# Optimization experiments

Measured on AMD Instinct MI355X. Metric: run time of the kernel, lower is better.

The kernel has to match this reference:

```python
import jax, jax.numpy as jnp
import numpy as np

N = 100000      # nodes
E = 1600000     # edges (avg degree 16)
G = 64          # graphs in batch
IN_DIM, HID, C2, C3, HEADS, NCLS = 64, 128, 64, 32, 4, 5
EPS = 1e-5
NEG_SLOPE = 0.2


def setup_inputs() -> dict:
    key = jax.random.key(0)
    ks = jax.random.split(key, 32)

    def w(k, fan_in, shape):
        return jax.random.normal(k, shape, dtype=jnp.float32) * (1.0 / np.sqrt(fan_in))

    x = jax.random.normal(ks[0], (N, IN_DIM), dtype=jnp.float32)
    edge_index = jax.random.randint(ks[1], (2, E), 0, N)
    batch = jnp.sort(jax.random.randint(ks[2], (N,), 0, G))

    inp = {"x": x, "edge_index": edge_index, "batch": batch}
    # GCN layers (PyG GCNConv: weight then symmetric-normalized aggregation, bias after)
    inp.update(W1=w(ks[3], IN_DIM, (IN_DIM, HID)), b1=jnp.zeros((HID,), jnp.float32))
    inp.update(W2=w(ks[4], HID, (HID, C2)), b2=jnp.zeros((C2,), jnp.float32))
    inp.update(W3=w(ks[5], C2, (C2, C3)), b3=jnp.zeros((C3,), jnp.float32))
    # BatchNorm (inference: running stats)
    def bn_params(k, d):
        k1, k2, k3 = jax.random.split(k, 3)
        return (1.0 + 0.1 * jax.random.normal(k1, (d,), jnp.float32),
                0.1 * jax.random.normal(k2, (d,), jnp.float32),
                0.1 * jax.random.normal(k3, (d,), jnp.float32),
                jax.random.uniform(k, (d,), jnp.float32, 0.5, 1.5))
    inp["g1"], inp["be1"], inp["m1"], inp["v1"] = bn_params(ks[6], HID)
    inp["g2"], inp["be2"], inp["m2"], inp["v2"] = bn_params(ks[7], C2)
    inp["g3"], inp["be3"], inp["m3"], inp["v3"] = bn_params(ks[8], C3)
    # GAT (heads=4, out=32, concat=False -> mean over heads)
    inp["Wg"] = w(ks[9], C3, (C3, HEADS * C3))
    inp["ag_s"] = w(ks[10], C3, (HEADS, C3))
    inp["ag_d"] = w(ks[11], C3, (HEADS, C3))
    inp["bg"] = jnp.zeros((C3,), jnp.float32)
    # classifier MLP 32 -> 16 -> 5
    inp["Wc1"] = w(ks[12], C3, (C3, 16)); inp["bc1"] = jnp.zeros((16,), jnp.float32)
    inp["Wc2"] = w(ks[13], 16, (16, NCLS)); inp["bc2"] = jnp.zeros((NCLS,), jnp.float32)
    return inp


def _bn(h, g, be, m, v):
    return (h - m) * jax.lax.rsqrt(v + EPS) * g + be


def reference(x, edge_index, batch,
              W1, b1, g1, be1, m1, v1,
              W2, b2, g2, be2, m2, v2,
              W3, b3, g3, be3, m3, v3,
              Wg, ag_s, ag_d, bg,
              Wc1, bc1, Wc2, bc2):
    n = x.shape[0]
    loop = jnp.arange(n)
    src = jnp.concatenate([edge_index[0], loop])  # add self-loops (PyG default)
    dst = jnp.concatenate([edge_index[1], loop])

    # GCN symmetric normalization: deg from dst (col), norm = d^-1/2[src]*d^-1/2[dst]
    deg = jnp.zeros((n,), x.dtype).at[dst].add(1.0)
    dinv = jax.lax.rsqrt(deg)  # deg >= 1 due to self-loops
    norm = (dinv[src] * dinv[dst])[:, None]

    def gcn(h, W, b):
        h = h @ W
        return jax.ops.segment_sum(h[src] * norm, dst, num_segments=n) + b

    h = jax.nn.relu(_bn(gcn(x, W1, b1), g1, be1, m1, v1))
    h = jax.nn.relu(_bn(gcn(h, W2, b2), g2, be2, m2, v2))
    h = jax.nn.relu(_bn(gcn(h, W3, b3), g3, be3, m3, v3))

    # GAT: per-edge attention, segment softmax over incoming edges per dst
    hh = (h @ Wg).reshape(n, HEADS, C3)          # [N,H,D]
    a_s = jnp.einsum('nhd,hd->nh', hh, ag_s)     # [N,H]
    a_d = jnp.einsum('nhd,hd->nh', hh, ag_d)
    e = jax.nn.leaky_relu(a_s[src] + a_d[dst], NEG_SLOPE)  # [Eall,H]
    emax = jax.lax.stop_gradient(jax.ops.segment_max(e, dst, num_segments=n))
    ee = jnp.exp(e - emax[dst])
    den = jax.ops.segment_sum(ee, dst, num_segments=n)
    att = ee / den[dst]                          # [Eall,H]
    agg = jax.ops.segment_sum(att[:, :, None] * hh[src], dst, num_segments=n)
    h = jax.nn.relu(agg.mean(axis=1) + bg)       # concat=False -> mean heads

    # global mean pool over graphs
    cnt = jax.ops.segment_sum(jnp.ones((n,), h.dtype), batch, num_segments=G)
    pooled = jax.ops.segment_sum(h, batch, num_segments=G) / jnp.maximum(cnt, 1.0)[:, None]

    # classifier (dropout inactive in eval)
    out = jax.nn.relu(pooled @ Wc1 + bc1) @ Wc2 + bc2
    return out
```

## Files before the change

### kernel.cpp

```cpp
#include <hip/hip_runtime.h>

#define EPSN   1e-5f
#define NEGS   0.2f
#define NGRAPH 64
#define BSHIFT 9
#define NPBK   512
#define GCAP   96

typedef _Float16 half_t;
typedef _Float16 halfv8 __attribute__((ext_vector_type(8)));
typedef _Float16 halfv4 __attribute__((ext_vector_type(4)));
typedef _Float16 halfv2 __attribute__((ext_vector_type(2)));

__device__ __forceinline__ float lrelu(float e) { return e > 0.f ? e : NEGS * e; }

__global__ void k_bin_count(const int* __restrict__ ed, int* __restrict__ bsize,
                            int E, int NB) {
    __shared__ int lcnt[1024];
    for (int i = threadIdx.x; i < NB; i += 256) lcnt[i] = 0;
    __syncthreads();
    int chunk = (E + gridDim.x - 1) / gridDim.x;
    int lo = blockIdx.x * chunk;
    int hi = min(E, lo + chunk);
    for (int e = lo + threadIdx.x; e < hi; e += 256)
        atomicAdd(&lcnt[ed[e] >> BSHIFT], 1);
    __syncthreads();
    for (int b = threadIdx.x; b < NB; b += 256)
        if (lcnt[b]) atomicAdd(&bsize[b], lcnt[b]);
}
__global__ void k_bucket_scan(const int* __restrict__ bsize, int* __restrict__ bbase,
                              int* __restrict__ gcur, int NB) {
    int lane = threadIdx.x;
    if (lane >= 64) return;
    int carry = 0;
    int rounds = (NB + 63) / 64;
    for (int r = 0; r < rounds; ++r) {
        int idx = r * 64 + lane;
        int orig = (idx < NB) ? bsize[idx] : 0;
        int v = orig;
#pragma unroll
        for (int o = 1; o < 64; o <<= 1) {
            int t = __shfl_up(v, o, 64);
            if (lane >= o) v += t;
        }
        if (idx < NB) {
            int excl = carry + v - orig;
            bbase[idx] = excl;
            gcur[idx] = excl;
        }
        carry += __shfl(v, 63, 64);
    }
}
__global__ void k_bin_write(const int* __restrict__ es, const int* __restrict__ ed,
                            int* __restrict__ gcur, unsigned* __restrict__ binned,
                            int E, int NB) {
    __shared__ int lcnt[1024];
    __shared__ int lofs[1024];
    int chunk = (E + gridDim.x - 1) / gridDim.x;
    int lo = blockIdx.x * chunk;
    int hi = min(E, lo + chunk);
    for (int i = threadIdx.x; i < NB; i += 256) lcnt[i] = 0;
    __syncthreads();
    for (int e = lo + threadIdx.x; e < hi; e += 256)
        atomicAdd(&lcnt[ed[e] >> BSHIFT], 1);
    __syncthreads();
    for (int b = threadIdx.x; b < NB; b += 256) {
        int c = lcnt[b];
        lofs[b] = c ? atomicAdd(&gcur[b], c) : 0;
    }
    __syncthreads();
    for (int i = threadIdx.x; i < NB; i += 256) lcnt[i] = 0;
    __syncthreads();
    for (int e = lo + threadIdx.x; e < hi; e += 256) {
        int s = es[e], t = ed[e];
        int b = t >> BSHIFT;
        int pos = lofs[b] + atomicAdd(&lcnt[b], 1);
        binned[pos] = ((unsigned)s << BSHIFT) | (unsigned)(t & (NPBK - 1));
    }
}
__global__ void k_csr_build(const unsigned* __restrict__ binned, const int* __restrict__ bbase,
                            const int* __restrict__ bsize, int* __restrict__ rowptr,
                            int* __restrict__ deg, float* __restrict__ dinv,
                            int* __restrict__ csrc, int N) {
    __shared__ int cnt_l[NPBK];
    __shared__ int ofs_l[NPBK];
    int b = blockIdx.x;
    int base = bbase[b];
    int cnt = bsize[b];
    int nlo = b << BSHIFT;
    int nhi = min(N, nlo + NPBK);
    int nv = nhi - nlo;
    int csrbase = base + nlo;
    int tid = threadIdx.x;
    for (int i = tid; i < NPBK; i += 256) cnt_l[i] = (i < nv) ? 1 : 0;
    __syncthreads();
    for (int e = tid; e < cnt; e += 256)
        atomicAdd(&cnt_l[binned[base + e] & (NPBK - 1)], 1);
    __syncthreads();
    if (tid < 64) {
        int carry = 0;
#pragma unroll
        for (int r = 0; r < NPBK / 64; ++r) {
            int idx = r * 64 + tid;
            int orig = cnt_l[idx];
            int v = orig;
#pragma unroll
            for (int o = 1; o < 64; o <<= 1) {
                int t = __shfl_up(v, o, 64);
                if (tid >= o) v += t;
            }
            ofs_l[idx] = carry + v - orig;
            carry += __shfl(v, 63, 64);
        }
    }
    __syncthreads();
    for (int i = tid; i < nv; i += 256) {
        int node = nlo + i;
        int d = cnt_l[i];
        rowptr[node] = csrbase + ofs_l[i];
        deg[node] = d;
        dinv[node] = rsqrtf((float)d);
    }
    __syncthreads();
    for (int i = tid; i < NPBK; i += 256) cnt_l[i] = ofs_l[i];
    __syncthreads();
    for (int e = tid; e < cnt; e += 256) {
        unsigned u = binned[base + e];
        int p = atomicAdd(&cnt_l[u & (NPBK - 1)], 1);
        csrc[csrbase + p] = (int)(u >> BSHIFT);
    }
    for (int i = tid; i < nv; i += 256) {
        int p = atomicAdd(&cnt_l[i], 1);
        csrc[csrbase + p] = nlo + i;
    }
}

__global__ void k_cvt_xh(const float* __restrict__ x, const float* __restrict__ dinv,
                         half_t* __restrict__ xh, int n) {
    int total = n * 8;
    for (int q = blockIdx.x * blockDim.x + threadIdx.x; q < total;
         q += gridDim.x * blockDim.x) {
        float din = dinv[q >> 3];
        float4 a = ((const float4*)x)[q * 2];
        float4 b = ((const float4*)x)[q * 2 + 1];
        halfv8 h;
        h[0] = (half_t)(a.x * din); h[1] = (half_t)(a.y * din);
        h[2] = (half_t)(a.z * din); h[3] = (half_t)(a.w * din);
        h[4] = (half_t)(b.x * din); h[5] = (half_t)(b.y * din);
        h[6] = (half_t)(b.z * din); h[7] = (half_t)(b.w * din);
        ((halfv8*)xh)[q] = h;
    }
}

template <int K, int M, int EPI>
__global__ void k_matmulh(const half_t* __restrict__ X, const float* __restrict__ W,
                          half_t* __restrict__ Y, int n,
                          const float* __restrict__ b, const float* __restrict__ g,
                          const float* __restrict__ be, const float* __restrict__ m,
                          const float* __restrict__ v, const float* __restrict__ dinv) {
    __shared__ float Wl[K * M];
    for (int i = threadIdx.x; i < K * M / 4; i += 256)
        ((float4*)Wl)[i] = ((const float4*)W)[i];
    __syncthreads();
    const int TPR = M / 4;
    const int RPB = 256 / TPR;
    const int c4  = (threadIdx.x % TPR) * 4;
    int row = blockIdx.x * RPB + threadIdx.x / TPR;
    if (row >= n) return;
    const halfv8* xr = (const halfv8*)(X + (long long)row * K);
    float4 acc = make_float4(0.f, 0.f, 0.f, 0.f);
#pragma unroll
    for (int k8 = 0; k8 < K / 8; ++k8) {
        halfv8 xv = xr[k8];
#pragma unroll
        for (int j = 0; j < 8; ++j) {
            float xs = (float)xv[j];
            float4 wv = *(const float4*)&Wl[(k8 * 8 + j) * M + c4];
            acc.x += xs * wv.x; acc.y += xs * wv.y;
            acc.z += xs * wv.z; acc.w += xs * wv.w;
        }
    }
    if (EPI == 1) {
        float4 bb = *(const float4*)(b + c4);
        float4 mm = *(const float4*)(m + c4);
        float4 vv = *(const float4*)(v + c4);
        float4 gg = *(const float4*)(g + c4);
        float4 ee = *(const float4*)(be + c4);
        acc.x = fmaxf((acc.x + bb.x - mm.x) * rsqrtf(vv.x + EPSN) * gg.x + ee.x, 0.f);
        acc.y = fmaxf((acc.y + bb.y - mm.y) * rsqrtf(vv.y + EPSN) * gg.y + ee.y, 0.f);
        acc.z = fmaxf((acc.z + bb.z - mm.z) * rsqrtf(vv.z + EPSN) * gg.z + ee.z, 0.f);
        acc.w = fmaxf((acc.w + bb.w - mm.w) * rsqrtf(vv.w + EPSN) * gg.w + ee.w, 0.f);
    } else {
        float din = dinv[row];
        acc.x *= din; acc.y *= din; acc.z *= din; acc.w *= din;
    }
    halfv4 hv;
    hv[0] = (half_t)acc.x; hv[1] = (half_t)acc.y;
    hv[2] = (half_t)acc.z; hv[3] = (half_t)acc.w;
    *(halfv4*)(Y + (long long)row * M + c4) = hv;
}

template <int M, int EPI>
__global__ void k_agg4h(const half_t* __restrict__ A, const int* __restrict__ rowptr,
                        const int* __restrict__ deg, const int* __restrict__ csrc,
                        const float* __restrict__ dinv,
                        const float* __restrict__ b, const float* __restrict__ g,
                        const float* __restrict__ be, const float* __restrict__ m,
                        const float* __restrict__ v,
                        half_t* __restrict__ B, int n) {
    const int LPE = M / 8;
    const int EPW = 64 / LPE;
    int node = blockIdx.x * 4 + (threadIdx.x >> 6);
    if (node >= n) return;
    int lane = threadIdx.x & 63;
    int eg = lane / LPE;
    int dl = lane % LPE;
    int beg = rowptr[node];
    int end = beg + deg[node];
    float acc[8];
#pragma unroll
    for (int j = 0; j < 8; ++j) acc[j] = 0.f;
    int i = beg + eg;
    for (; i + EPW < end; i += 2 * EPW) {
        int s0 = csrc[i];
        int s1 = csrc[i + EPW];
        halfv8 x0 = *(const halfv8*)(A + (long long)s0 * M + dl * 8);
        halfv8 x1 = *(const halfv8*)(A + (long long)s1 * M + dl * 8);
#pragma unroll
        for (int j = 0; j < 8; ++j) acc[j] += (float)x0[j] + (float)x1[j];
    }
    if (i < end) {
        int s = csrc[i];
        halfv8 xv = *(const halfv8*)(A + (long long)s * M + dl * 8);
#pragma unroll
        for (int j = 0; j < 8; ++j) acc[j] += (float)xv[j];
    }
#pragma unroll
    for (int off = LPE; off < 64; off <<= 1) {
#pragma unroll
        for (int j = 0; j < 8; ++j) acc[j] += __shfl_xor(acc[j], off);
    }
    if (eg == 0) {
        float din = dinv[node];
        int d0 = dl * 8;
        float o[8];
#pragma unroll
        for (int j = 0; j < 8; ++j) o[j] = acc[j] * din;
        if (EPI == 1) {
#pragma unroll
            for (int j = 0; j < 8; ++j) {
                int d = d0 + j;
                o[j] = fmaxf((o[j] + b[d] - m[d]) * rsqrtf(v[d] + EPSN) * g[d] + be[d], 0.f);
            }
        }
        halfv8 hw;
#pragma unroll
        for (int j = 0; j < 8; ++j) hw[j] = (half_t)o[j];
        *(halfv8*)(B + (long long)node * M + d0) = hw;
    }
}

__global__ void k_wsd(const float* __restrict__ Wg, const float* __restrict__ ags,
                      const float* __restrict__ agd, float* __restrict__ wsd) {
    int j = threadIdx.x;
    if (j < 128) {
        int k = j >> 2, h = j & 3;
        float ss = 0.f, dd = 0.f;
        for (int d2 = 0; d2 < 32; ++d2) {
            float wv = Wg[k * 128 + h * 32 + d2];
            ss += wv * ags[h * 32 + d2];
            dd += wv * agd[h * 32 + d2];
        }
        wsd[j] = ss;
        wsd[128 + j] = dd;
    }
}

__global__ void k_agg_att(const half_t* __restrict__ A, const int* __restrict__ rowptr,
                          const int* __restrict__ deg, const int* __restrict__ csrc,
                          const float* __restrict__ dinv,
                          const float* __restrict__ b, const float* __restrict__ g,
                          const float* __restrict__ be, const float* __restrict__ m,
                          const float* __restrict__ v, const float* __restrict__ wsd,
                          half_t* __restrict__ H3h, float* __restrict__ a_s,
                          float* __restrict__ a_d, int n) {
    __shared__ float Wl[256];
    for (int i = threadIdx.x; i < 256; i += 256) Wl[i] = wsd[i];
    __syncthreads();
    const int M = 32, EPW = 16;
    int node = blockIdx.x * 4 + (threadIdx.x >> 6);
    if (node >= n) return;
    int lane = threadIdx.x & 63;
    int eg = lane >> 2;
    int dl = lane & 3;
    int beg = rowptr[node];
    int end = beg + deg[node];
    float acc[8];
#pragma unroll
    for (int j = 0; j < 8; ++j) acc[j] = 0.f;
    int i = beg + eg;
    for (; i + EPW < end; i += 2 * EPW) {
        int s0 = csrc[i];
        int s1 = csrc[i + EPW];
        halfv8 x0 = *(const halfv8*)(A + (long long)s0 * M + dl * 8);
        halfv8 x1 = *(const halfv8*)(A + (long long)s1 * M + dl * 8);
#pragma unroll
        for (int j = 0; j < 8; ++j) acc[j] += (float)x0[j] + (float)x1[j];
    }
    if (i < end) {
        int s = csrc[i];
        halfv8 xv = *(const halfv8*)(A + (long long)s * M + dl * 8);
#pragma unroll
        for (int j = 0; j < 8; ++j) acc[j] += (float)xv[j];
    }
#pragma unroll
    for (int off = 4; off < 64; off <<= 1) {
#pragma unroll
        for (int j = 0; j < 8; ++j) acc[j] += __shfl_xor(acc[j], off);
    }
    float din = dinv[node];
    int d0 = dl * 8;
    float hv[8];
#pragma unroll
    for (int j = 0; j < 8; ++j) {
        int d = d0 + j;
        hv[j] = fmaxf((acc[j] * din + b[d] - m[d]) * rsqrtf(v[d] + EPSN) * g[d] + be[d], 0.f);
    }
    if (eg == 0) {
        halfv8 hw;
#pragma unroll
        for (int j = 0; j < 8; ++j) hw[j] = (half_t)hv[j];
        *(halfv8*)(H3h + (long long)node * M + d0) = hw;
    }
    int h = lane & 3, sel = (lane >> 2) & 1;
    const float* wp = &Wl[sel * 128];
    float o = 0.f;
#pragma unroll
    for (int src = 0; src < 4; ++src) {
#pragma unroll
        for (int j = 0; j < 8; ++j) {
            float xv = __shfl(hv[j], src);
            o += xv * wp[(src * 8 + j) * 4 + h];
        }
    }
    if (lane < 4) a_s[node * 4 + h] = o;
    else if (lane < 8) a_d[node * 4 + h] = o;
}

__global__ void k_gat4(const half_t* __restrict__ H3h, const float* __restrict__ a_s,
                       const float* __restrict__ a_d, const int* __restrict__ rowptr,
                       const int* __restrict__ deg, const int* __restrict__ csrc,
                       const float* __restrict__ Wg, const float* __restrict__ bg,
                       float* __restrict__ H4, int n) {
    __shared__ float sc[4][GCAP * 4];
    __shared__ int   srcb[4][GCAP];
    __shared__ float wb[4][128];
    int w = threadIdx.x >> 6;
    int node = blockIdx.x * 4 + w;
    if (node >= n) return;
    int lane = threadIdx.x & 63;
    int beg = rowptr[node];
    int cnt = deg[node];
    bool fits = (cnt <= GCAP);
    float4 ad4 = ((const float4*)a_d)[node];
    float m0 = -1e30f, m1 = -1e30f, m2 = -1e30f, m3 = -1e30f;
    if (fits) {
        for (int e = lane; e < cnt; e += 64) {
            int s = csrc[beg + e];
            srcb[w][e] = s;
            float4 as = ((const float4*)a_s)[s];
            float e0 = lrelu(as.x + ad4.x);
            float e1 = lrelu(as.y + ad4.y);
            float e2 = lrelu(as.z + ad4.z);
            float e3 = lrelu(as.w + ad4.w);
            *(float4*)&sc[w][e * 4] = make_float4(e0, e1, e2, e3);
            m0 = fmaxf(m0, e0); m1 = fmaxf(m1, e1);
            m2 = fmaxf(m2, e2); m3 = fmaxf(m3, e3);
        }
    } else {
        for (int e = lane; e < cnt; e += 64) {
            int s = csrc[beg + e];
            float4 as = ((const float4*)a_s)[s];
            m0 = fmaxf(m0, lrelu(as.x + ad4.x));
            m1 = fmaxf(m1, lrelu(as.y + ad4.y));
            m2 = fmaxf(m2, lrelu(as.z + ad4.z));
            m3 = fmaxf(m3, lrelu(as.w + ad4.w));
        }
    }
#pragma unroll
    for (int o = 1; o < 64; o <<= 1) {
        m0 = fmaxf(m0, __shfl_xor(m0, o));
        m1 = fmaxf(m1, __shfl_xor(m1, o));
        m2 = fmaxf(m2, __shfl_xor(m2, o));
        m3 = fmaxf(m3, __shfl_xor(m3, o));
    }
    float s0 = 0.f, s1 = 0.f, s2 = 0.f, s3 = 0.f;
    if (fits) {
        for (int e = lane; e < cnt; e += 64) {
            float4 sv = *(float4*)&sc[w][e * 4];
            float p0 = __expf(sv.x - m0);
            float p1 = __expf(sv.y - m1);
            float p2 = __expf(sv.z - m2);
            float p3 = __expf(sv.w - m3);
            *(float4*)&sc[w][e * 4] = make_float4(p0, p1, p2, p3);
            s0 += p0; s1 += p1; s2 += p2; s3 += p3;
        }
    } else {
        for (int e = lane; e < cnt; e += 64) {
            int s = csrc[beg + e];
            float4 as = ((const float4*)a_s)[s];
            s0 += __expf(lrelu(as.x + ad4.x) - m0);
            s1 += __expf(lrelu(as.y + ad4.y) - m1);
            s2 += __expf(lrelu(as.z + ad4.z) - m2);
            s3 += __expf(lrelu(as.w + ad4.w) - m3);
        }
    }
#pragma unroll
    for (int o = 1; o < 64; o <<= 1) {
        s0 += __shfl_xor(s0, o);
        s1 += __shfl_xor(s1, o);
        s2 += __shfl_xor(s2, o);
        s3 += __shfl_xor(s3, o);
    }
    float inv0 = 0.25f / s0, inv1 = 0.25f / s1, inv2 = 0.25f / s2, inv3 = 0.25f / s3;
    int q = lane >> 4;
    int k = lane & 15;
    float acc[8];
#pragma unroll
    for (int j = 0; j < 8; ++j) acc[j] = 0.f;
    if (fits) {
        int i = q;
        for (; i + 4 < cnt; i += 8) {
            int sA = srcb[w][i];
            int sB = srcb[w][i + 4];
            halfv2 xA = *(const halfv2*)(H3h + (long long)sA * 32 + 2 * k);
            halfv2 xB = *(const halfv2*)(H3h + (long long)sB * 32 + 2 * k);
            float4 wA = *(float4*)&sc[w][i * 4];
            float4 wB = *(float4*)&sc[w][(i + 4) * 4];
            float a0 = (float)xA[0], a1 = (float)xA[1];
            float b0 = (float)xB[0], b1 = (float)xB[1];
            acc[0] += wA.x * a0 + wB.x * b0; acc[1] += wA.x * a1 + wB.x * b1;
            acc[2] += wA.y * a0 + wB.y * b0; acc[3] += wA.y * a1 + wB.y * b1;
            acc[4] += wA.z * a0 + wB.z * b0; acc[5] += wA.z * a1 + wB.z * b1;
            acc[6] += wA.w * a0 + wB.w * b0; acc[7] += wA.w * a1 + wB.w * b1;
        }
        if (i < cnt) {
            int s = srcb[w][i];
            halfv2 xv = *(const halfv2*)(H3h + (long long)s * 32 + 2 * k);
            float4 wv = *(float4*)&sc[w][i * 4];
            float x0 = (float)xv[0], x1 = (float)xv[1];
            acc[0] += wv.x * x0; acc[1] += wv.x * x1;
            acc[2] += wv.y * x0; acc[3] += wv.y * x1;
            acc[4] += wv.z * x0; acc[5] += wv.z * x1;
            acc[6] += wv.w * x0; acc[7] += wv.w * x1;
        }
    } else {
        for (int i = q; i < cnt; i += 4) {
            int s = csrc[beg + i];
            float4 as = ((const float4*)a_s)[s];
            float p0 = __expf(lrelu(as.x + ad4.x) - m0);
            float p1 = __expf(lrelu(as.y + ad4.y) - m1);
            float p2 = __expf(lrelu(as.z + ad4.z) - m2);
            float p3 = __expf(lrelu(as.w + ad4.w) - m3);
            halfv2 xv = *(const halfv2*)(H3h + (long long)s * 32 + 2 * k);
            float x0 = (float)xv[0], x1 = (float)xv[1];
            acc[0] += p0 * x0; acc[1] += p0 * x1;
            acc[2] += p1 * x0; acc[3] += p1 * x1;
            acc[4] += p2 * x0; acc[5] += p2 * x1;
            acc[6] += p3 * x0; acc[7] += p3 * x1;
        }
    }
#pragma unroll
    for (int o = 16; o < 64; o <<= 1) {
#pragma unroll
        for (int j = 0; j < 8; ++j) acc[j] += __shfl_xor(acc[j], o);
    }
    if (q == 0) {
        float invh[4] = {inv0, inv1, inv2, inv3};
#pragma unroll
        for (int h = 0; h < 4; ++h) {
            wb[w][h * 32 + 2 * k]     = acc[h * 2]     * invh[h];
            wb[w][h * 32 + 2 * k + 1] = acc[h * 2 + 1] * invh[h];
        }
    }
    int d = lane & 31;
    int h0 = lane >> 5;
    int half_ = h0 * 64;
    float o = 0.f;
#pragma unroll
    for (int j = 0; j < 64; ++j) {
        int jj = half_ + j;
        o += wb[w][jj] * Wg[(jj & 31) * 128 + (jj >> 5) * 32 + d];
    }
    o += __shfl_xor(o, 32);
    if (lane < 32)
        H4[(long long)node * 32 + d] = fmaxf(o + bg[d], 0.f);
}

__global__ void k_pool_init(float* __restrict__ pooled, float* __restrict__ cnt) {
    int i = blockIdx.x * blockDim.x + threadIdx.x;
    if (i < NGRAPH * 32) pooled[i] = 0.f;
    if (i < NGRAPH) cnt[i] = 0.f;
}
__global__ void k_pool2(const float* __restrict__ h, const int* __restrict__ batch,
                        float* __restrict__ pooled, float* __restrict__ cnt, int n) {
    __shared__ float lp[NGRAPH * 32];
    __shared__ float lc[NGRAPH];
    int tid = threadIdx.x;
    for (int i = tid; i < NGRAPH * 32; i += 256) lp[i] = 0.f;
    for (int i = tid; i < NGRAPH; i += 256) lc[i] = 0.f;
    __syncthreads();
    int per = (n + gridDim.x - 1) / gridDim.x;
    int lo = blockIdx.x * per;
    int hi = min(n, lo + per);
    for (long long i = (long long)lo * 32 + tid; i < (long long)hi * 32; i += 256) {
        int ni = (int)(i >> 5), dd = (int)(i & 31);
        int b = batch[ni];
        atomicAdd(&lp[b * 32 + dd], h[i]);
        if (dd == 0) atomicAdd(&lc[b], 1.f);
    }
    __syncthreads();
    for (int i = tid; i < NGRAPH * 32; i += 256)
        if (lp[i] != 0.f) atomicAdd(&pooled[i], lp[i]);
    for (int i = tid; i < NGRAPH; i += 256)
        if (lc[i] != 0.f) atomicAdd(&cnt[i], lc[i]);
}

__global__ void k_classifier(const float* __restrict__ pooled, const float* __restrict__ cnt,
                             const float* __restrict__ Wc1, const float* __restrict__ bc1,
                             const float* __restrict__ Wc2, const float* __restrict__ bc2,
                             float* __restrict__ out) {
    __shared__ float pl[NGRAPH * 32];
    __shared__ float t1[NGRAPH * 16];
    int tid = threadIdx.x;
    for (int i = tid; i < NGRAPH * 32; i += blockDim.x) {
        int g = i >> 5;
        pl[i] = pooled[i] / fmaxf(cnt[g], 1.f);
    }
    __syncthreads();
    for (int i = tid; i < NGRAPH * 16; i += blockDim.x) {
        int g = i >> 4, c = i & 15;
        float acc = bc1[c];
#pragma unroll
        for (int d = 0; d < 32; ++d) acc += pl[g * 32 + d] * Wc1[d * 16 + c];
        t1[i] = fmaxf(acc, 0.f);
    }
    __syncthreads();
    for (int i = tid; i < NGRAPH * 5; i += blockDim.x) {
        int g = i / 5, c = i % 5;
        float acc = bc2[c];
#pragma unroll
        for (int k = 0; k < 16; ++k) acc += t1[g * 16 + k] * Wc2[k * 5 + c];
        out[i] = acc;
    }
}

static inline dim3 gsz(long long work, int block = 256) {
    long long g = (work + block - 1) / block;
    if (g > 262144) g = 262144;
    if (g < 1) g = 1;
    return dim3((unsigned)g);
}

extern "C" void kernel_launch(void* const* d_in, const int* in_sizes, int n_in,
                              void* d_out, int out_size, void* d_ws, size_t ws_size,
                              hipStream_t stream) {
    const float* x     = (const float*)d_in[0];
    const int*   ei    = (const int*)d_in[1];
    const int*   batch = (const int*)d_in[2];
    const float* W1 = (const float*)d_in[3];  const float* b1 = (const float*)d_in[4];
    const float* W2 = (const float*)d_in[5];  const float* b2 = (const float*)d_in[6];
    const float* W3 = (const float*)d_in[7];  const float* b3 = (const float*)d_in[8];
    const float* g1 = (const float*)d_in[9];  const float* be1 = (const float*)d_in[10];
    const float* m1 = (const float*)d_in[11]; const float* v1  = (const float*)d_in[12];
    const float* g2 = (const float*)d_in[13]; const float* be2 = (const float*)d_in[14];
    const float* m2 = (const float*)d_in[15]; const float* v2  = (const float*)d_in[16];
    const float* g3 = (const float*)d_in[17]; const float* be3 = (const float*)d_in[18];
    const float* m3 = (const float*)d_in[19]; const float* v3  = (const float*)d_in[20];
    const float* Wg  = (const float*)d_in[21];
    const float* ags = (const float*)d_in[22];
    const float* agd = (const float*)d_in[23];
    const float* bg  = (const float*)d_in[24];
    const float* Wc1 = (const float*)d_in[25]; const float* bc1 = (const float*)d_in[26];
    const float* Wc2 = (const float*)d_in[27]; const float* bc2 = (const float*)d_in[28];
    float* out = (float*)d_out;

    const int N = in_sizes[0] / 64;
    const int E = in_sizes[1] / 2;
    const int* esrc = ei;
    const int* edst = ei + E;
    const int NB = (N + NPBK - 1) >> BSHIFT;

    size_t off = 0;
    auto take = [&](size_t bytes) -> void* {
        void* p = (char*)d_ws + off;
        off += bytes;
        off = (off + 255) & ~(size_t)255;
        return p;
    };
    int*    deg    = (int*)take((size_t)N * 4);
    float*  dinv   = (float*)take((size_t)N * 4);
    int*    rowptr = (int*)take((size_t)N * 4);
    int*    bsize  = (int*)take((size_t)1024 * 4);
    int*    bbase  = (int*)take((size_t)1024 * 4);
    int*    gcur   = (int*)take((size_t)1024 * 4);
    float*  wsd    = (float*)take((size_t)256 * 4);
    int*    csrc   = (int*)take((size_t)(E + N) * 4);
    half_t* bufAh  = (half_t*)take((size_t)N * 64 * 2);
    half_t* bufBh  = (half_t*)take((size_t)N * 64 * 2);
    float*  bufC   = (float*)take((size_t)N * 128 * 4);
    half_t* h3h    = (half_t*)take((size_t)N * 32 * 2);
    float*  a_s    = (float*)take((size_t)N * 4 * 4);
    float*  a_d    = (float*)take((size_t)N * 4 * 4);
    float*  pooled = (float*)take((size_t)NGRAPH * 32 * 4);
    float*  cnt    = (float*)take((size_t)NGRAPH * 4);
    unsigned* binned = (unsigned*)bufC;
    half_t* H1h    = (half_t*)bufC;
    float*  H4     = (float*)bufAh;
    (void)ws_size; (void)n_in; (void)out_size;

    const dim3 B256(256);

    hipMemsetAsync(bsize, 0, (size_t)NB * 4, stream);
    hipLaunchKernelGGL(k_bin_count, dim3(512), B256, 0, stream, edst, bsize, E, NB);
    hipLaunchKernelGGL(k_bucket_scan, dim3(1), dim3(64), 0, stream, bsize, bbase, gcur, NB);
    hipLaunchKernelGGL(k_bin_write, dim3(512), B256, 0, stream, esrc, edst, gcur, binned, E, NB);
    hipLaunchKernelGGL(k_csr_build, dim3(NB), B256, 0, stream,
                       binned, bbase, bsize, rowptr, deg, dinv, csrc, N);
    hipLaunchKernelGGL(k_wsd, dim3(1), dim3(128), 0, stream, Wg, ags, agd, wsd);

    hipLaunchKernelGGL(k_cvt_xh, gsz((long long)N * 8), B256, 0, stream, x, dinv, bufAh, N);
    hipLaunchKernelGGL((k_agg4h<64, 0>), dim3((N + 3) / 4), B256, 0, stream,
                       bufAh, rowptr, deg, csrc, dinv,
                       nullptr, nullptr, nullptr, nullptr, nullptr, bufBh, N);
    hipLaunchKernelGGL((k_matmulh<64, 128, 1>), dim3((N + 7) / 8), B256, 0, stream,
                       bufBh, W1, H1h, N, b1, g1, be1, m1, v1, nullptr);
    hipLaunchKernelGGL((k_matmulh<128, 64, 2>), dim3((N + 15) / 16), B256, 0, stream,
                       H1h, W2, bufAh, N, nullptr, nullptr, nullptr, nullptr, nullptr, dinv);
    hipLaunchKernelGGL((k_agg4h<64, 1>), dim3((N + 3) / 4), B256, 0, stream,
                       bufAh, rowptr, deg, csrc, dinv, b2, g2, be2, m2, v2, bufBh, N);
    hipLaunchKernelGGL((k_matmulh<64, 32, 2>), dim3((N + 31) / 32), B256, 0, stream,
                       bufBh, W3, bufAh, N, nullptr, nullptr, nullptr, nullptr, nullptr, dinv);
    hipLaunchKernelGGL(k_agg_att, dim3((N + 3) / 4), B256, 0, stream,
                       bufAh, rowptr, deg, csrc, dinv, b3, g3, be3, m3, v3,
                       wsd, h3h, a_s, a_d, N);

    hipLaunchKernelGGL(k_gat4, dim3((N + 3) / 4), B256, 0, stream,
                       h3h, a_s, a_d, rowptr, deg, csrc, Wg, bg, H4, N);

    hipLaunchKernelGGL(k_pool_init, dim3(9), B256, 0, stream, pooled, cnt);
    hipLaunchKernelGGL(k_pool2, dim3(128), B256, 0, stream, H4, batch, pooled, cnt, N);
    hipLaunchKernelGGL(k_classifier, dim3(1), B256, 0, stream, pooled, cnt, Wc1, bc1, Wc2, bc2, out);
}
```

Measured before the change: 601.6 us.

## Store layer-3 features in software FP8 and fuse mean pooling into GAT

The layer-3 pre-aggregation features and the post-BN H3 features move from fp16 to a software-encoded E4M3 byte format, which halves the gather bytes in the agg_att and GAT kernels at the cost of extra ALU work to decode and encode. The separate H4 buffer and pooling kernels are removed. The GAT kernel now atomically accumulates into 64 partitioned pooled buffers, which a small reduce kernel sums afterwards. FP8 lowers accuracy and could exceed tolerance, and the pool partitions require an extra memset.

```diff
diff --git a/kernel.cpp b/kernel.cpp
--- a/kernel.cpp
+++ b/kernel.cpp
@@ -6,13 +6,49 @@
 #define BSHIFT 9
 #define NPBK   512
 #define GCAP   96
+#define NPART  64
+#define PSTR   (NGRAPH * 32 + NGRAPH)
 
 typedef _Float16 half_t;
 typedef _Float16 halfv8 __attribute__((ext_vector_type(8)));
 typedef _Float16 halfv4 __attribute__((ext_vector_type(4)));
-typedef _Float16 halfv2 __attribute__((ext_vector_type(2)));
 
 __device__ __forceinline__ float lrelu(float e) { return e > 0.f ? e : NEGS * e; }
+
+__device__ __forceinline__ float fp8_dec(unsigned b) {
+    unsigned s = b >> 7;
+    unsigned e = (b >> 3) & 15;
+    unsigned m = b & 7;
+    float v = (e == 0) ? (float)m * 0.001953125f
+                       : __uint_as_float(((e + 120u) << 23) | (m << 20));
+    return s ? -v : v;
+}
+__device__ __forceinline__ unsigned fp8_enc(float x) {
+    unsigned bits = __float_as_uint(x);
+    unsigned s = bits >> 31;
+    float a = fabsf(x);
+    a = fminf(a, 448.0f);
+    unsigned abits = __float_as_uint(a);
+    int ef = (int)(abits >> 23) - 127;
+    if (ef < -10) return s << 7;
+    int ulpe = ((ef < -6) ? -6 : ef) - 3;
+    float scale  = __uint_as_float((unsigned)(127 - ulpe) << 23);
+    float iscale = __uint_as_float((unsigned)(127 + ulpe) << 23);
+    float r = rintf(a * scale);
+    float q = fminf(r * iscale, 448.f);
+    unsigned qb = __float_as_uint(q);
+    int eq = (int)(qb >> 23) - 127;
+    unsigned e8, m8;
+    if (eq < -6) {
+        unsigned ri = (unsigned)r;
+        e8 = (ri >= 8) ? 1u : 0u;
+        m8 = (ri >= 8) ? 0u : ri;
+    } else {
+        e8 = (unsigned)(eq + 7);
+        m8 = (qb >> 20) & 7;
+    }
+    return (s << 7) | (e8 << 3) | m8;
+}
 
 __global__ void k_bin_count(const int* __restrict__ ed, int* __restrict__ bsize,
                             int E, int NB) {
@@ -198,6 +234,38 @@
     hv[0] = (half_t)acc.x; hv[1] = (half_t)acc.y;
     hv[2] = (half_t)acc.z; hv[3] = (half_t)acc.w;
     *(halfv4*)(Y + (long long)row * M + c4) = hv;
+}
+
+template <int K, int M>
+__global__ void k_matmul_fp8(const half_t* __restrict__ X, const float* __restrict__ W,
+                             unsigned char* __restrict__ Y, int n,
+                             const float* __restrict__ dinv) {
+    __shared__ float Wl[K * M];
+    for (int i = threadIdx.x; i < K * M / 4; i += 256)
+        ((float4*)Wl)[i] = ((const float4*)W)[i];
+    __syncthreads();
+    const int TPR = M / 4;
+    const int RPB = 256 / TPR;
+    const int c4  = (threadIdx.x % TPR) * 4;
+    int row = blockIdx.x * RPB + threadIdx.x / TPR;
+    if (row >= n) return;
+    const halfv8* xr = (const halfv8*)(X + (long long)row * K);
+    float4 acc = make_float4(0.f, 0.f, 0.f, 0.f);
+#pragma unroll
+    for (int k8 = 0; k8 < K / 8; ++k8) {
+        halfv8 xv = xr[k8];
+#pragma unroll
+        for (int j = 0; j < 8; ++j) {
+            float xs = (float)xv[j];
+            float4 wv = *(const float4*)&Wl[(k8 * 8 + j) * M + c4];
+            acc.x += xs * wv.x; acc.y += xs * wv.y;
+            acc.z += xs * wv.z; acc.w += xs * wv.w;
+        }
+    }
+    float din = dinv[row];
+    unsigned u = fp8_enc(acc.x * din) | (fp8_enc(acc.y * din) << 8) |
+                 (fp8_enc(acc.z * din) << 16) | (fp8_enc(acc.w * din) << 24);
+    *(unsigned*)(Y + (long long)row * M + c4) = u;
 }
 
 template <int M, int EPI>
@@ -276,13 +344,13 @@
     }
 }
 
-__global__ void k_agg_att(const half_t* __restrict__ A, const int* __restrict__ rowptr,
+__global__ void k_agg_att(const unsigned char* __restrict__ A, const int* __restrict__ rowptr,
                           const int* __restrict__ deg, const int* __restrict__ csrc,
                           const float* __restrict__ dinv,
                           const float* __restrict__ b, const float* __restrict__ g,
                           const float* __restrict__ be, const float* __restrict__ m,
                           const float* __restrict__ v, const float* __restrict__ wsd,
-                          half_t* __restrict__ H3h, float* __restrict__ a_s,
+                          unsigned char* __restrict__ H3f8, float* __restrict__ a_s,
                           float* __restrict__ a_d, int n) {
     __shared__ float Wl[256];
     for (int i = threadIdx.x; i < 256; i += 256) Wl[i] = wsd[i];
@@ -302,16 +370,22 @@
     for (; i + EPW < end; i += 2 * EPW) {
         int s0 = csrc[i];
         int s1 = csrc[i + EPW];
-        halfv8 x0 = *(const halfv8*)(A + (long long)s0 * M + dl * 8);
-        halfv8 x1 = *(const halfv8*)(A + (long long)s1 * M + dl * 8);
-#pragma unroll
-        for (int j = 0; j < 8; ++j) acc[j] += (float)x0[j] + (float)x1[j];
+        uint2 u0 = *(const uint2*)(A + (long long)s0 * M + dl * 8);
+        uint2 u1 = *(const uint2*)(A + (long long)s1 * M + dl * 8);
+#pragma unroll
+        for (int j = 0; j < 4; ++j) {
+            acc[j]     += fp8_dec((u0.x >> (8 * j)) & 255) + fp8_dec((u1.x >> (8 * j)) & 255);
+            acc[4 + j] += fp8_dec((u0.y >> (8 * j)) & 255) + fp8_dec((u1.y >> (8 * j)) & 255);
+        }
     }
     if (i < end) {
         int s = csrc[i];
-        halfv8 xv = *(const halfv8*)(A + (long long)s * M + dl * 8);
-#pragma unroll
-        for (int j = 0; j < 8; ++j) acc[j] += (float)xv[j];
+        uint2 u = *(const uint2*)(A + (long long)s * M + dl * 8);
+#pragma unroll
+        for (int j = 0; j < 4; ++j) {
+            acc[j]     += fp8_dec((u.x >> (8 * j)) & 255);
+            acc[4 + j] += fp8_dec((u.y >> (8 * j)) & 255);
+        }
     }
 #pragma unroll
     for (int off = 4; off < 64; off <<= 1) {
@@ -327,10 +401,11 @@
         hv[j] = fmaxf((acc[j] * din + b[d] - m[d]) * rsqrtf(v[d] + EPSN) * g[d] + be[d], 0.f);
     }
     if (eg == 0) {
-        halfv8 hw;
-#pragma unroll
-        for (int j = 0; j < 8; ++j) hw[j] = (half_t)hv[j];
-        *(halfv8*)(H3h + (long long)node * M + d0) = hw;
+        unsigned lo = fp8_enc(hv[0]) | (fp8_enc(hv[1]) << 8) |
+                      (fp8_enc(hv[2]) << 16) | (fp8_enc(hv[3]) << 24);
+        unsigned hi = fp8_enc(hv[4]) | (fp8_enc(hv[5]) << 8) |
+                      (fp8_enc(hv[6]) << 16) | (fp8_enc(hv[7]) << 24);
+        *(uint2*)(H3f8 + (long long)node * M + d0) = make_uint2(lo, hi);
     }
     int h = lane & 3, sel = (lane >> 2) & 1;
     const float* wp = &Wl[sel * 128];
@@ -347,11 +422,12 @@
     else if (lane < 8) a_d[node * 4 + h] = o;
 }
 
-__global__ void k_gat4(const half_t* __restrict__ H3h, const float* __restrict__ a_s,
+__global__ void k_gat4(const unsigned char* __restrict__ H3f8, const float* __restrict__ a_s,
                        const float* __restrict__ a_d, const int* __restrict__ rowptr,
                        const int* __restrict__ deg, const int* __restrict__ csrc,
                        const float* __restrict__ Wg, const float* __restrict__ bg,
-                       float* __restrict__ H4, int n) {
+                       const int* __restrict__ batch, float* __restrict__ pooled_part,
+                       int n) {
     __shared__ float sc[4][GCAP * 4];
     __shared__ int   srcb[4][GCAP];
     __shared__ float wb[4][128];
@@ -433,12 +509,12 @@
         for (; i + 4 < cnt; i += 8) {
             int sA = srcb[w][i];
             int sB = srcb[w][i + 4];
-            halfv2 xA = *(const halfv2*)(H3h + (long long)sA * 32 + 2 * k);
-            halfv2 xB = *(const halfv2*)(H3h + (long long)sB * 32 + 2 * k);
+            unsigned vA = *(const unsigned short*)(H3f8 + (long long)sA * 32 + 2 * k);
+            unsigned vB = *(const unsigned short*)(H3f8 + (long long)sB * 32 + 2 * k);
             float4 wA = *(float4*)&sc[w][i * 4];
             float4 wB = *(float4*)&sc[w][(i + 4) * 4];
-            float a0 = (float)xA[0], a1 = (float)xA[1];
-            float b0 = (float)xB[0], b1 = (float)xB[1];
+            float a0 = fp8_dec(vA & 255), a1 = fp8_dec(vA >> 8);
+            float b0 = fp8_dec(vB & 255), b1 = fp8_dec(vB >> 8);
             acc[0] += wA.x * a0 + wB.x * b0; acc[1] += wA.x * a1 + wB.x * b1;
             acc[2] += wA.y * a0 + wB.y * b0; acc[3] += wA.y * a1 + wB.y * b1;
             acc[4] += wA.z * a0 + wB.z * b0; acc[5] += wA.z * a1 + wB.z * b1;
@@ -446,9 +522,9 @@
         }
         if (i < cnt) {
             int s = srcb[w][i];
-            halfv2 xv = *(const halfv2*)(H3h + (long long)s * 32 + 2 * k);
+            unsigned v = *(const unsigned short*)(H3f8 + (long long)s * 32 + 2 * k);
             float4 wv = *(float4*)&sc[w][i * 4];
-            float x0 = (float)xv[0], x1 = (float)xv[1];
+            float x0 = fp8_dec(v & 255), x1 = fp8_dec(v >> 8);
             acc[0] += wv.x * x0; acc[1] += wv.x * x1;
             acc[2] += wv.y * x0; acc[3] += wv.y * x1;
             acc[4] += wv.z * x0; acc[5] += wv.z * x1;
@@ -462,8 +538,8 @@
             float p1 = __expf(lrelu(as.y + ad4.y) - m1);
             float p2 = __expf(lrelu(as.z + ad4.z) - m2);
             float p3 = __expf(lrelu(as.w + ad4.w) - m3);
-            halfv2 xv = *(const halfv2*)(H3h + (long long)s * 32 + 2 * k);
-            float x0 = (float)xv[0], x1 = (float)xv[1];
+            unsigned v = *(const unsigned short*)(H3f8 + (long long)s * 32 + 2 * k);
+            float x0 = fp8_dec(v & 255), x1 = fp8_dec(v >> 8);
             acc[0] += p0 * x0; acc[1] += p0 * x1;
             acc[2] += p1 * x0; acc[3] += p1 * x1;
             acc[4] += p2 * x0; acc[5] += p2 * x1;
@@ -493,37 +569,22 @@
         o += wb[w][jj] * Wg[(jj & 31) * 128 + (jj >> 5) * 32 + d];
     }
     o += __shfl_xor(o, 32);
-    if (lane < 32)
-        H4[(long long)node * 32 + d] = fmaxf(o + bg[d], 0.f);
-}
-
-__global__ void k_pool_init(float* __restrict__ pooled, float* __restrict__ cnt) {
+    if (lane < 32) {
+        float val = fmaxf(o + bg[d], 0.f);
+        int g = batch[node];
+        float* pp = pooled_part + (size_t)(blockIdx.x & (NPART - 1)) * PSTR;
+        atomicAdd(&pp[g * 32 + d], val);
+        if (d == 0) atomicAdd(&pp[NGRAPH * 32 + g], 1.f);
+    }
+}
+
+__global__ void k_pool_reduce(const float* __restrict__ part, float* __restrict__ outp) {
     int i = blockIdx.x * blockDim.x + threadIdx.x;
-    if (i < NGRAPH * 32) pooled[i] = 0.f;
-    if (i < NGRAPH) cnt[i] = 0.f;
-}
-__global__ void k_pool2(const float* __restrict__ h, const int* __restrict__ batch,
-                        float* __restrict__ pooled, float* __restrict__ cnt, int n) {
-    __shared__ float lp[NGRAPH * 32];
-    __shared__ float lc[NGRAPH];
-    int tid = threadIdx.x;
-    for (int i = tid; i < NGRAPH * 32; i += 256) lp[i] = 0.f;
-    for (int i = tid; i < NGRAPH; i += 256) lc[i] = 0.f;
-    __syncthreads();
-    int per = (n + gridDim.x - 1) / gridDim.x;
-    int lo = blockIdx.x * per;
-    int hi = min(n, lo + per);
-    for (long long i = (long long)lo * 32 + tid; i < (long long)hi * 32; i += 256) {
-        int ni = (int)(i >> 5), dd = (int)(i & 31);
-        int b = batch[ni];
-        atomicAdd(&lp[b * 32 + dd], h[i]);
-        if (dd == 0) atomicAdd(&lc[b], 1.f);
-    }
-    __syncthreads();
-    for (int i = tid; i < NGRAPH * 32; i += 256)
-        if (lp[i] != 0.f) atomicAdd(&pooled[i], lp[i]);
-    for (int i = tid; i < NGRAPH; i += 256)
-        if (lc[i] != 0.f) atomicAdd(&cnt[i], lc[i]);
+    if (i >= PSTR) return;
+    float s = 0.f;
+#pragma unroll 8
+    for (int c = 0; c < NPART; ++c) s += part[(size_t)c * PSTR + i];
+    outp[i] = s;
 }
 
 __global__ void k_classifier(const float* __restrict__ pooled, const float* __restrict__ cnt,
@@ -609,19 +670,21 @@
     half_t* bufAh  = (half_t*)take((size_t)N * 64 * 2);
     half_t* bufBh  = (half_t*)take((size_t)N * 64 * 2);
     float*  bufC   = (float*)take((size_t)N * 128 * 4);
-    half_t* h3h    = (half_t*)take((size_t)N * 32 * 2);
+    unsigned char* h3f8 = (unsigned char*)take((size_t)N * 32);
     float*  a_s    = (float*)take((size_t)N * 4 * 4);
     float*  a_d    = (float*)take((size_t)N * 4 * 4);
-    float*  pooled = (float*)take((size_t)NGRAPH * 32 * 4);
-    float*  cnt    = (float*)take((size_t)NGRAPH * 4);
+    float*  ppart  = (float*)take((size_t)NPART * PSTR * 4);
+    float*  pooled = (float*)take((size_t)PSTR * 4);
+    float*  cnt    = pooled + NGRAPH * 32;
     unsigned* binned = (unsigned*)bufC;
     half_t* H1h    = (half_t*)bufC;
-    float*  H4     = (float*)bufAh;
+    unsigned char* a3f8 = (unsigned char*)bufAh;
     (void)ws_size; (void)n_in; (void)out_size;
 
     const dim3 B256(256);
 
     hipMemsetAsync(bsize, 0, (size_t)NB * 4, stream);
+    hipMemsetAsync(ppart, 0, (size_t)NPART * PSTR * 4, stream);
     hipLaunchKernelGGL(k_bin_count, dim3(512), B256, 0, stream, edst, bsize, E, NB);
     hipLaunchKernelGGL(k_bucket_scan, dim3(1), dim3(64), 0, stream, bsize, bbase, gcur, NB);
     hipLaunchKernelGGL(k_bin_write, dim3(512), B256, 0, stream, esrc, edst, gcur, binned, E, NB);
@@ -639,16 +702,15 @@
                        H1h, W2, bufAh, N, nullptr, nullptr, nullptr, nullptr, nullptr, dinv);
     hipLaunchKernelGGL((k_agg4h<64, 1>), dim3((N + 3) / 4), B256, 0, stream,
                        bufAh, rowptr, deg, csrc, dinv, b2, g2, be2, m2, v2, bufBh, N);
-    hipLaunchKernelGGL((k_matmulh<64, 32, 2>), dim3((N + 31) / 32), B256, 0, stream,
-                       bufBh, W3, bufAh, N, nullptr, nullptr, nullptr, nullptr, nullptr, dinv);
+    hipLaunchKernelGGL((k_matmul_fp8<64, 32>), dim3((N + 31) / 32), B256, 0, stream,
+                       bufBh, W3, a3f8, N, dinv);
     hipLaunchKernelGGL(k_agg_att, dim3((N + 3) / 4), B256, 0, stream,
-                       bufAh, rowptr, deg, csrc, dinv, b3, g3, be3, m3, v3,
-                       wsd, h3h, a_s, a_d, N);
+                       a3f8, rowptr, deg, csrc, dinv, b3, g3, be3, m3, v3,
+                       wsd, h3f8, a_s, a_d, N);
 
     hipLaunchKernelGGL(k_gat4, dim3((N + 3) / 4), B256, 0, stream,
-                       h3h, a_s, a_d, rowptr, deg, csrc, Wg, bg, H4, N);
-
-    hipLaunchKernelGGL(k_pool_init, dim3(9), B256, 0, stream, pooled, cnt);
-    hipLaunchKernelGGL(k_pool2, dim3(128), B256, 0, stream, H4, batch, pooled, cnt, N);
+                       h3f8, a_s, a_d, rowptr, deg, csrc, Wg, bg, batch, ppart, N);
+
+    hipLaunchKernelGGL(k_pool_reduce, dim3((PSTR + 255) / 256), B256, 0, stream, ppart, pooled);
     hipLaunchKernelGGL(k_classifier, dim3(1), B256, 0, stream, pooled, cnt, Wc1, bc1, Wc2, bc2, out);
 }
```

Measured after the change: 1.029 ms. +71.0%, slower.

## Fuse global mean pooling into GAT kernel via partitioned atomic partial sums

Applied to the files above, without the earlier changes.

The GAT kernel no longer writes the per-node H4 output. Each node's result is atomically added into one of 64 partitioned partial-sum buffers selected by block index, along with the node counts. A small reduction kernel then sums the partitions before the classifier. This removes the H4 round trip through global memory and the separate pool init and pool kernels, in exchange for many global atomics that may contend, since batch is sorted and neighbouring nodes hit the same graph slots.

```diff
diff --git a/kernel.cpp b/kernel.cpp
--- a/kernel.cpp
+++ b/kernel.cpp
@@ -6,6 +6,8 @@
 #define BSHIFT 9
 #define NPBK   512
 #define GCAP   96
+#define NPART  64
+#define PSTR   (NGRAPH * 32 + NGRAPH)
 
 typedef _Float16 half_t;
 typedef _Float16 halfv8 __attribute__((ext_vector_type(8)));
@@ -351,7 +353,8 @@
                        const float* __restrict__ a_d, const int* __restrict__ rowptr,
                        const int* __restrict__ deg, const int* __restrict__ csrc,
                        const float* __restrict__ Wg, const float* __restrict__ bg,
-                       float* __restrict__ H4, int n) {
+                       const int* __restrict__ batch, float* __restrict__ pooled_part,
+                       int n) {
     __shared__ float sc[4][GCAP * 4];
     __shared__ int   srcb[4][GCAP];
     __shared__ float wb[4][128];
@@ -493,37 +496,22 @@
         o += wb[w][jj] * Wg[(jj & 31) * 128 + (jj >> 5) * 32 + d];
     }
     o += __shfl_xor(o, 32);
-    if (lane < 32)
-        H4[(long long)node * 32 + d] = fmaxf(o + bg[d], 0.f);
-}
-
-__global__ void k_pool_init(float* __restrict__ pooled, float* __restrict__ cnt) {
+    if (lane < 32) {
+        float val = fmaxf(o + bg[d], 0.f);
+        int g = batch[node];
+        float* pp = pooled_part + (size_t)(blockIdx.x & (NPART - 1)) * PSTR;
+        atomicAdd(&pp[g * 32 + d], val);
+        if (d == 0) atomicAdd(&pp[NGRAPH * 32 + g], 1.f);
+    }
+}
+
+__global__ void k_pool_reduce(const float* __restrict__ part, float* __restrict__ outp) {
     int i = blockIdx.x * blockDim.x + threadIdx.x;
-    if (i < NGRAPH * 32) pooled[i] = 0.f;
-    if (i < NGRAPH) cnt[i] = 0.f;
-}
-__global__ void k_pool2(const float* __restrict__ h, const int* __restrict__ batch,
-                        float* __restrict__ pooled, float* __restrict__ cnt, int n) {
-    __shared__ float lp[NGRAPH * 32];
-    __shared__ float lc[NGRAPH];
-    int tid = threadIdx.x;
-    for (int i = tid; i < NGRAPH * 32; i += 256) lp[i] = 0.f;
-    for (int i = tid; i < NGRAPH; i += 256) lc[i] = 0.f;
-    __syncthreads();
-    int per = (n + gridDim.x - 1) / gridDim.x;
-    int lo = blockIdx.x * per;
-    int hi = min(n, lo + per);
-    for (long long i = (long long)lo * 32 + tid; i < (long long)hi * 32; i += 256) {
-        int ni = (int)(i >> 5), dd = (int)(i & 31);
-        int b = batch[ni];
-        atomicAdd(&lp[b * 32 + dd], h[i]);
-        if (dd == 0) atomicAdd(&lc[b], 1.f);
-    }
-    __syncthreads();
-    for (int i = tid; i < NGRAPH * 32; i += 256)
-        if (lp[i] != 0.f) atomicAdd(&pooled[i], lp[i]);
-    for (int i = tid; i < NGRAPH; i += 256)
-        if (lc[i] != 0.f) atomicAdd(&cnt[i], lc[i]);
+    if (i >= PSTR) return;
+    float s = 0.f;
+#pragma unroll 8
+    for (int c = 0; c < NPART; ++c) s += part[(size_t)c * PSTR + i];
+    outp[i] = s;
 }
 
 __global__ void k_classifier(const float* __restrict__ pooled, const float* __restrict__ cnt,
@@ -612,16 +600,17 @@
     half_t* h3h    = (half_t*)take((size_t)N * 32 * 2);
     float*  a_s    = (float*)take((size_t)N * 4 * 4);
     float*  a_d    = (float*)take((size_t)N * 4 * 4);
-    float*  pooled = (float*)take((size_t)NGRAPH * 32 * 4);
-    float*  cnt    = (float*)take((size_t)NGRAPH * 4);
+    float*  ppart  = (float*)take((size_t)NPART * PSTR * 4);
+    float*  pooled = (float*)take((size_t)PSTR * 4);
+    float*  cnt    = pooled + NGRAPH * 32;
     unsigned* binned = (unsigned*)bufC;
     half_t* H1h    = (half_t*)bufC;
-    float*  H4     = (float*)bufAh;
     (void)ws_size; (void)n_in; (void)out_size;
 
     const dim3 B256(256);
 
     hipMemsetAsync(bsize, 0, (size_t)NB * 4, stream);
+    hipMemsetAsync(ppart, 0, (size_t)NPART * PSTR * 4, stream);
     hipLaunchKernelGGL(k_bin_count, dim3(512), B256, 0, stream, edst, bsize, E, NB);
     hipLaunchKernelGGL(k_bucket_scan, dim3(1), dim3(64), 0, stream, bsize, bbase, gcur, NB);
     hipLaunchKernelGGL(k_bin_write, dim3(512), B256, 0, stream, esrc, edst, gcur, binned, E, NB);
@@ -646,9 +635,8 @@
                        wsd, h3h, a_s, a_d, N);
 
     hipLaunchKernelGGL(k_gat4, dim3((N + 3) / 4), B256, 0, stream,
-                       h3h, a_s, a_d, rowptr, deg, csrc, Wg, bg, H4, N);
-
-    hipLaunchKernelGGL(k_pool_init, dim3(9), B256, 0, stream, pooled, cnt);
-    hipLaunchKernelGGL(k_pool2, dim3(128), B256, 0, stream, H4, batch, pooled, cnt, N);
+                       h3h, a_s, a_d, rowptr, deg, csrc, Wg, bg, batch, ppart, N);
+
+    hipLaunchKernelGGL(k_pool_reduce, dim3((PSTR + 255) / 256), B256, 0, stream, ppart, pooled);
     hipLaunchKernelGGL(k_classifier, dim3(1), B256, 0, stream, pooled, cnt, Wc1, bc1, Wc2, bc2, out);
 }
```

New measurement: 572.1 us. -4.9%, faster.
